# Performance work log

Measured on AMD Instinct MI355X. Metric: run time of the kernel, lower is better.

Reference implementation:

```python
import jax, jax.numpy as jnp
import numpy as np

B, I, T, H, O = 256, 128, 256, 512, 2
EPS = 1e-5  # BatchNorm1d default eps


def setup_inputs() -> dict:
    key = jax.random.key(0)
    ks = jax.random.split(key, 32)
    stdv = 1.0 / np.sqrt(H)
    u = lambda k, shape: jax.random.uniform(k, shape, jnp.float32, -stdv, stdv)
    X = jax.random.normal(ks[0], (B, I, T), jnp.float32)
    Mask = (jax.random.uniform(ks[1], (B, I, T)) > 0.5).astype(jnp.float32)
    Delta = jax.random.uniform(ks[2], (B, I, T)) * 5.0
    inp = jnp.stack([X, Mask, Delta], axis=1)  # [B, 3, I, T]
    return dict(
        input=inp,
        x_mean=jnp.float32(0.0),
        W_dg_x=u(ks[3], (I, I)), b_dg_x=u(ks[4], (I,)),
        W_dg_h=u(ks[5], (I, H)), b_dg_h=u(ks[6], (H,)),
        W_xz=u(ks[7], (I, H)), W_hz=u(ks[8], (H, H)), W_mz=u(ks[9], (I, H)), b_z=u(ks[10], (H,)),
        W_xr=u(ks[11], (I, H)), W_hr=u(ks[12], (H, H)), W_mr=u(ks[13], (I, H)), b_r=u(ks[14], (H,)),
        W_xh=u(ks[15], (I, H)), W_hh=u(ks[16], (H, H)), W_mh=u(ks[17], (I, H)), b_h=u(ks[18], (H,)),
        W_hy=u(ks[19], (H, O)), b_hy=u(ks[20], (O,)),
        bn_gamma=u(ks[21], (H,)), bn_beta=u(ks[22], (H,)),
    )


def reference(input, x_mean, W_dg_x, b_dg_x, W_dg_h, b_dg_h,
              W_xz, W_hz, W_mz, b_z, W_xr, W_hr, W_mr, b_r,
              W_xh, W_hh, W_mh, b_h, W_hy, b_hy, bn_gamma, bn_beta):
    # input: [B, 3, I, T] -> time-major [T, B, I]
    Xs = jnp.transpose(input[:, 0], (2, 0, 1))
    Ms = jnp.transpose(input[:, 1], (2, 0, 1))
    Ds = jnp.transpose(input[:, 2], (2, 0, 1))
    b, i = input.shape[0], input.shape[2]
    h0 = jnp.zeros((b, W_hz.shape[0]), input.dtype)       # Hidden_State buffer (zeros, broadcast over batch)
    xl0 = jnp.zeros((b, i), input.dtype)                   # X_last_obs buffer

    def step(carry, xs):
        h, x_last = carry
        x, m, d = xs
        gamma_x = jnp.exp(-jax.nn.relu(d @ W_dg_x + b_dg_x))   # [B, I]
        gamma_h = jnp.exp(-jax.nn.relu(d @ W_dg_h + b_dg_h))   # [B, H]
        x_last = jnp.where(m > 0, x, x_last)
        x = m * x + (1 - m) * (gamma_x * x_last + (1 - gamma_x) * x_mean)
        h = gamma_h * h
        z = jax.nn.sigmoid(x @ W_xz + h @ W_hz + m @ W_mz + b_z)
        r = jax.nn.sigmoid(x @ W_xr + h @ W_hr + m @ W_mr + b_r)
        h_tilde = jnp.tanh(x @ W_xh + (r * h) @ W_hh + m @ W_mh + b_h)
        h = (1 - z) * h + z * h_tilde
        # BatchNorm1d in training mode: batch mean, biased variance
        mu = h.mean(axis=0)
        var = ((h - mu) ** 2).mean(axis=0)
        h = bn_gamma * (h - mu) * jax.lax.rsqrt(var + EPS) + bn_beta
        y = jax.nn.softplus(h @ W_hy + b_hy)
        return (h, x_last), (y, h)

    _, (ys, hs) = jax.lax.scan(step, (h0, xl0), (Xs, Ms, Ds))
    # back to batch-major [B, T, *]
    return jnp.transpose(ys, (1, 0, 2)), jnp.transpose(hs, (1, 0, 2))
```

## Files before the change

kernel.cpp:

```cpp
#include <hip/hip_runtime.h>
#include <math.h>

#define Bb 256
#define Ii 128
#define Tt 256
#define Hh 512
#define Oo 2
#define TBr (Tt*Bb)
#define EPS_BN 1e-5f

typedef __attribute__((ext_vector_type(8))) short short8;
typedef __attribute__((ext_vector_type(8))) __bf16 bf16x8;
typedef __attribute__((ext_vector_type(4))) float f32x4;
typedef __attribute__((ext_vector_type(2))) float f32x2;
typedef unsigned long long u64;

__device__ __forceinline__ f32x4 mfma_bf16(short8 a, short8 b, f32x4 c) {
    return __builtin_amdgcn_mfma_f32_16x16x32_bf16(
        __builtin_bit_cast(bf16x8, a), __builtin_bit_cast(bf16x8, b), c, 0, 0, 0);
}
__device__ __forceinline__ short f2bf(float f) {
    union { float f; unsigned u; } v; v.f = f;
    unsigned r = (v.u + 0x7FFFu + ((v.u >> 16) & 1u)) >> 16;
    return (short)r;
}
__device__ __forceinline__ float bf2f(short s) {
    union { unsigned u; float f; } v; v.u = ((unsigned)(unsigned short)s) << 16;
    return v.f;
}
__device__ __forceinline__ float sigmoidf_(float x) { return 1.f / (1.f + expf(-x)); }
__device__ __forceinline__ float softplusf_(float x) { return fmaxf(x, 0.f) + log1pf(expf(-fabsf(x))); }

#define ALD_F(p)  __hip_atomic_load((p),  __ATOMIC_RELAXED, __HIP_MEMORY_SCOPE_AGENT)
#define AST_F(p,v) __hip_atomic_store((p), (v), __ATOMIC_RELAXED, __HIP_MEMORY_SCOPE_AGENT)
#define AADD_F(p,v) (void)__hip_atomic_fetch_add((p), (v), __ATOMIC_RELAXED, __HIP_MEMORY_SCOPE_AGENT)

__device__ __forceinline__ short8 ald16(const short* p) {
    union { u64 u[2]; short8 s; } v;
    v.u[0] = ALD_F((const u64*)p);
    v.u[1] = ALD_F((const u64*)(p + 4));
    return v.s;
}
__device__ __forceinline__ u64 pack4bf(float a, float b, float c_, float d) {
    return (u64)(unsigned short)f2bf(a)
         | ((u64)(unsigned short)f2bf(b) << 16)
         | ((u64)(unsigned short)f2bf(c_) << 32)
         | ((u64)(unsigned short)f2bf(d) << 48);
}

__global__ __launch_bounds__(1024) void repack_kernel(const float* __restrict__ in,
                                                      float* __restrict__ Xall,
                                                      short* __restrict__ Mall,
                                                      short* __restrict__ Dall)
{
    __shared__ float tile[32][33];
    const int bz = blockIdx.z;
    const int b = bz / 3, cch = bz % 3;
    const int t0 = blockIdx.x * 32, i0 = blockIdx.y * 32;
    const int tx = threadIdx.x, ty = threadIdx.y;
    const float* src = in + ((size_t)b * 3 + cch) * (size_t)Ii * Tt;
    tile[ty][tx] = src[(size_t)(i0 + ty) * Tt + t0 + tx];
    __syncthreads();
    const float v = tile[tx][ty];
    const size_t off = ((size_t)(t0 + ty) * Bb + b) * Ii + i0 + tx;
    if (cch == 0)      Xall[off] = v;
    else if (cch == 1) Mall[off] = f2bf(v);
    else               Dall[off] = f2bf(v);
}

__global__ __launch_bounds__(256) void pack_weights_kernel(
    const float* __restrict__ W_dg_x, const float* __restrict__ W_dg_h,
    const float* __restrict__ W_xz, const float* __restrict__ W_hz, const float* __restrict__ W_mz, const float* __restrict__ b_z,
    const float* __restrict__ W_xr, const float* __restrict__ W_hr, const float* __restrict__ W_mr, const float* __restrict__ b_r,
    const float* __restrict__ W_xh, const float* __restrict__ W_hh, const float* __restrict__ W_mh,
    short* __restrict__ Wc1T, short* __restrict__ Wc2T,
    short* __restrict__ WdgxT, short* __restrict__ WdghT, float* __restrict__ bias1)
{
    const int idx = blockIdx.x * blockDim.x + threadIdx.x;
    const int n1 = 1024 * 768, n2 = 512 * 768, n3 = 128 * 128, n4 = 512 * 128;
    if (idx < n1) {
        const int n = idx / 768, k = idx % 768;
        const int col = (n < Hh) ? n : (n - Hh);
        const float* Wx = (n < Hh) ? W_xz : W_xr;
        const float* Wm = (n < Hh) ? W_mz : W_mr;
        const float* Wh = (n < Hh) ? W_hz : W_hr;
        float v;
        if (k < Ii)        v = Wx[(size_t)k * Hh + col];
        else if (k < 2*Ii) v = Wm[(size_t)(k - Ii) * Hh + col];
        else               v = Wh[(size_t)(k - 2*Ii) * Hh + col];
        Wc1T[idx] = f2bf(v);
    } else if (idx < n1 + n2) {
        const int j = idx - n1;
        const int n = j / 768, k = j % 768;
        float v;
        if (k < Ii)        v = W_xh[(size_t)k * Hh + n];
        else if (k < 2*Ii) v = W_mh[(size_t)(k - Ii) * Hh + n];
        else               v = W_hh[(size_t)(k - 2*Ii) * Hh + n];
        Wc2T[j] = f2bf(v);
    } else if (idx < n1 + n2 + n3) {
        const int j = idx - n1 - n2;
        const int n = j >> 7, k = j & 127;
        WdgxT[j] = f2bf(W_dg_x[(size_t)k * Ii + n]);
    } else if (idx < n1 + n2 + n3 + n4) {
        const int j = idx - n1 - n2 - n3;
        const int n = j >> 7, k = j & 127;
        WdghT[j] = f2bf(W_dg_h[(size_t)k * Hh + n]);
    } else if (idx < n1 + n2 + n3 + n4 + 1024) {
        const int n = idx - n1 - n2 - n3 - n4;
        bias1[n] = (n < Hh) ? b_z[n] : b_r[n - Hh];
    }
}

__global__ __launch_bounds__(64) void gdecay_kernel(const short* __restrict__ A,
                                                    const short* __restrict__ BT,
                                                    const float* __restrict__ bias,
                                                    short* __restrict__ C, int N)
{
    const int lane = threadIdx.x;
    const int c = lane & 15, g = lane >> 4;
    const int m0 = blockIdx.x * 32, n0 = blockIdx.y * 64;
    const short* a0 = A + (size_t)(m0 + c) * Ii + 8 * g;
    const short* a1 = a0 + (size_t)16 * Ii;
    const short* bw = BT + (size_t)(n0 + c) * Ii + 8 * g;
    f32x4 acc[2][4];
    #pragma unroll
    for (int i = 0; i < 2; ++i)
        #pragma unroll
        for (int f = 0; f < 4; ++f) acc[i][f] = (f32x4){0.f, 0.f, 0.f, 0.f};
    #pragma unroll
    for (int k0 = 0; k0 < 128; k0 += 32) {
        const short8 av0 = *(const short8*)(a0 + k0);
        const short8 av1 = *(const short8*)(a1 + k0);
        #pragma unroll
        for (int fn = 0; fn < 4; ++fn) {
            const short8 bv = *(const short8*)(bw + (size_t)fn * 16 * Ii + k0);
            acc[0][fn] = mfma_bf16(av0, bv, acc[0][fn]);
            acc[1][fn] = mfma_bf16(av1, bv, acc[1][fn]);
        }
    }
    #pragma unroll
    for (int fn = 0; fn < 4; ++fn) {
        const int n = n0 + fn * 16 + c;
        const float bs = bias[n];
        #pragma unroll
        for (int fm = 0; fm < 2; ++fm) {
            #pragma unroll
            for (int j = 0; j < 4; ++j) {
                const int m = m0 + fm * 16 + 4 * g + j;
                const float v = expf(-fmaxf(acc[fm][fn][j] + bs, 0.f));
                C[(size_t)m * N + n] = f2bf(v);
            }
        }
    }
}

__global__ __launch_bounds__(256) void xeff_scan_kernel(const float* __restrict__ Xall,
                                                        const short* __restrict__ Mall,
                                                        const short* __restrict__ Gx,
                                                        const float* __restrict__ xmean_p,
                                                        short* __restrict__ Xe)
{
    const int bi = blockIdx.x * blockDim.x + threadIdx.x;
    if (bi >= Bb * Ii) return;
    const float xm = xmean_p[0];
    float xl = 0.f;
    for (int t = 0; t < Tt; ++t) {
        const size_t off = (size_t)t * Bb * Ii + bi;
        const float x = Xall[off];
        const float m = bf2f(Mall[off]);
        const float gx = bf2f(Gx[off]);
        if (m > 0.f) xl = x;
        Xe[off] = f2bf(m * x + (1.f - m) * (gx * xl + (1.f - gx) * xm));
    }
}

#define XM_STR 264
#define HP_STR 520
#define GH_STR 520

__global__ __launch_bounds__(512, 1) void grud_persistent(
    const short* __restrict__ Xe, const short* __restrict__ Ma,
    const short* __restrict__ Ghb,
    const short* __restrict__ Wc1T, const short* __restrict__ Wc2T,
    const float* __restrict__ bias1, const float* __restrict__ b_h,
    const float* __restrict__ bn_g, const float* __restrict__ bn_b,
    const float* __restrict__ Why, const float* __restrict__ bhy,
    short* __restrict__ rhG,
    short* __restrict__ HrawG,
    float* __restrict__ PstSum,
    int* __restrict__ f1,
    int* __restrict__ f2,
    float* __restrict__ out_hs, float* __restrict__ out_ys)
{
    const int bid = blockIdx.x, tid = threadIdx.x;
    const int w = tid >> 6, lane = tid & 63, c = lane & 15, g = lane >> 4;
    const int mt = bid & 15, ng = bid >> 4;
    const int m0 = mt * 16;

    __shared__ short sXM[16 * XM_STR];
    __shared__ short sHP[16 * HP_STR];
    __shared__ short sGH[16 * GH_STR];
    __shared__ float sZ[32 * 17];
    __shared__ float scratch[1536];
    __shared__ float sWhy[1024];
    __shared__ float scs[512], shs[512];
    __shared__ float ysred[16];

    sWhy[tid] = Why[tid]; sWhy[tid + 512] = Why[tid + 512];
    const float bhy0 = bhy[0], bhy1 = bhy[1];

    const int colt = w & 3, kh = w >> 2;
    const int colbaseA = (colt < 2) ? (ng * 32 + colt * 16)
                                    : (512 + ng * 32 + (colt - 2) * 16);
    short8 wA[12];
    {
        const short* bw = Wc1T + (size_t)(colbaseA + c) * 768 + kh * 384 + 8 * g;
        #pragma unroll
        for (int s = 0; s < 12; ++s) wA[s] = *(const short8*)(bw + 32 * s);
    }
    const int colt2 = w & 1, kq = w >> 1;
    const int colbaseB = ng * 32 + colt2 * 16;
    short8 wB[6];
    {
        const short* bw = Wc2T + (size_t)(colbaseB + c) * 768 + kq * 192 + 8 * g;
        #pragma unroll
        for (int s = 0; s < 6; ++s) wB[s] = *(const short8*)(bw + 32 * s);
    }
    {
        const int r = tid >> 5, cu = tid & 31;
        const short* src = (cu < 16)
            ? (Xe + ((size_t)(m0 + r)) * Ii + 8 * cu)
            : (Ma + ((size_t)(m0 + r)) * Ii + 8 * (cu - 16));
        *(short8*)(&sXM[r * XM_STR + 8 * cu]) = *(const short8*)src;
    }
    __syncthreads();

    for (int t = 0; t < Tt; ++t) {
        f32x4 accA = (f32x4){0.f, 0.f, 0.f, 0.f};
        f32x4 accB = (f32x4){0.f, 0.f, 0.f, 0.f};
        if (kh == 0) {
            #pragma unroll
            for (int s = 0; s < 8; ++s)
                accA = mfma_bf16(wA[s],
                    *(const short8*)(&sXM[c * XM_STR + 32 * s + 8 * g]), accA);
        }
        #pragma unroll
        for (int s = 0; s < 6; ++s) {
            const int k = kq * 192 + 32 * s;
            if (k < 256)
                accB = mfma_bf16(wB[s],
                    *(const short8*)(&sXM[c * XM_STR + k + 8 * g]), accB);
        }

        if (t > 0) {
            const int pR = (t + 2) % 3;
            {
                const float s1 = ALD_F(&PstSum[pR * 1024 + tid]);
                const float s2 = ALD_F(&PstSum[pR * 1024 + 512 + tid]);
                const float mu = s1 * (1.f / 256.f);
                const float var = fmaxf(s2 * (1.f / 256.f) - mu * mu, 0.f);
                const float sc = bn_g[tid] * rsqrtf(var + EPS_BN);
                scs[tid] = sc; shs[tid] = bn_b[tid] - mu * sc;
            }
            __syncthreads();
            float p0 = 0.f, p1 = 0.f;
            #pragma unroll
            for (int i = 0; i < 4; ++i) {
                const int idx = tid + i * 512;
                const int r = idx >> 7, c4 = (idx & 127) * 4;
                union { u64 u; unsigned short us[4]; } hv, gv;
                hv.u = ALD_F((const u64*)(HrawG + (size_t)(m0 + r) * Hh + c4));
                gv.u = *(const u64*)(&sGH[r * GH_STR + c4]);
                float h[4];
                #pragma unroll
                for (int j = 0; j < 4; ++j)
                    h[j] = fmaf(bf2f((short)hv.us[j]), scs[c4 + j], shs[c4 + j]);
                *(u64*)(&sHP[r * HP_STR + c4]) =
                    pack4bf(h[0] * bf2f((short)gv.us[0]), h[1] * bf2f((short)gv.us[1]),
                            h[2] * bf2f((short)gv.us[2]), h[3] * bf2f((short)gv.us[3]));
                if ((c4 >> 5) == ng) {
                    *(f32x4*)(&out_hs[((size_t)(m0 + r) * Tt + (t - 1)) * Hh + c4]) =
                        (f32x4){h[0], h[1], h[2], h[3]};
                }
                if (r == ng) {
                    #pragma unroll
                    for (int j = 0; j < 4; ++j) {
                        p0 = fmaf(h[j], sWhy[2 * (c4 + j)], p0);
                        p1 = fmaf(h[j], sWhy[2 * (c4 + j) + 1], p1);
                    }
                }
            }
            #pragma unroll
            for (int s = 1; s < 64; s <<= 1) { p0 += __shfl_xor(p0, s); p1 += __shfl_xor(p1, s); }
            if (lane == 0) { ysred[2 * w] = p0; ysred[2 * w + 1] = p1; }
            __syncthreads();
            if (tid == 0) {
                float q0 = 0.f, q1 = 0.f;
                #pragma unroll
                for (int i = 0; i < 8; ++i) { q0 += ysred[2 * i]; q1 += ysred[2 * i + 1]; }
                out_ys[((size_t)(m0 + ng) * Tt + (t - 1)) * Oo + 0] = softplusf_(q0 + bhy0);
                out_ys[((size_t)(m0 + ng) * Tt + (t - 1)) * Oo + 1] = softplusf_(q1 + bhy1);
            }
        } else {
            #pragma unroll
            for (int i = 0; i < 4; ++i) {
                const int idx = tid + i * 512;
                const int r = idx >> 7, c4 = (idx & 127) * 4;
                *(u64*)(&sHP[r * HP_STR + c4]) = 0ull;
            }
            __syncthreads();
        }

        if (kh == 0) {
            #pragma unroll
            for (int s = 8; s < 12; ++s)
                accA = mfma_bf16(wA[s],
                    *(const short8*)(&sHP[c * HP_STR + (32 * s - 256) + 8 * g]), accA);
        } else {
            #pragma unroll
            for (int s = 0; s < 12; ++s)
                accA = mfma_bf16(wA[s],
                    *(const short8*)(&sHP[c * HP_STR + 128 + 32 * s + 8 * g]), accA);
        }
        if (kh == 1) {
            float* sp = scratch + (colt * 64 + lane) * 4;
            sp[0] = accA[0]; sp[1] = accA[1]; sp[2] = accA[2]; sp[3] = accA[3];
        }
        __syncthreads();
        if (kh == 0) {
            const float* sp = scratch + (colt * 64 + lane) * 4;
            accA[0] += sp[0]; accA[1] += sp[1]; accA[2] += sp[2]; accA[3] += sp[3];
            if (colt < 2) {
                #pragma unroll
                for (int j = 0; j < 4; ++j) {
                    const int lc = colt * 16 + 4 * g + j;
                    const float v = sigmoidf_(accA[j] + bias1[ng * 32 + lc]);
                    sZ[lc * 17 + c] = v;
                }
            } else {
                const int nn0 = ng * 32 + (colt - 2) * 16 + 4 * g;
                float rv[4];
                #pragma unroll
                for (int j = 0; j < 4; ++j) {
                    const float v = sigmoidf_(accA[j] + bias1[512 + nn0 + j]);
                    rv[j] = v * bf2f(sHP[c * HP_STR + nn0 + j]);
                }
                AST_F((u64*)(rhG + ((size_t)(m0 + c) * Hh + nn0)),
                      pack4bf(rv[0], rv[1], rv[2], rv[3]));
            }
        }
        __syncthreads();
        if (tid == 0) AST_F(&f1[bid * 16], t + 1);
        if (t + 1 < Tt) {
            #pragma unroll
            for (int i = 0; i < 4; ++i) {
                const int idx = tid + i * 512;
                const int r = idx >> 7, c4 = (idx & 127) * 4;
                const u64 v = *(const u64*)(Ghb + ((size_t)(t + 1) * Bb + m0 + r) * Hh + c4);
                *(u64*)(&sGH[r * GH_STR + c4]) = v;
            }
        }
        if (tid < 4) AST_F(&PstSum[((t + 1) % 3) * 1024 + bid * 4 + tid], 0.f);
        if (tid < 16) {
            while (__hip_atomic_load(&f1[(mt + 16 * tid) * 16],
                                     __ATOMIC_RELAXED, __HIP_MEMORY_SCOPE_AGENT) < t + 1)
                __builtin_amdgcn_s_sleep(1);
        }
        __syncthreads();

        #pragma unroll
        for (int s = 0; s < 6; ++s) {
            const int k = kq * 192 + 32 * s;
            if (k >= 256)
                accB = mfma_bf16(wB[s],
                    ald16(rhG + (size_t)(m0 + c) * Hh + (k - 256) + 8 * g), accB);
        }
        if (kq > 0) {
            float* sp = scratch + ((colt2 * 3 + kq - 1) * 64 + lane) * 4;
            sp[0] = accB[0]; sp[1] = accB[1]; sp[2] = accB[2]; sp[3] = accB[3];
        }
        __syncthreads();
        if (kq == 0) {
            #pragma unroll
            for (int qq = 0; qq < 3; ++qq) {
                const float* sp = scratch + ((colt2 * 3 + qq) * 64 + lane) * 4;
                accB[0] += sp[0]; accB[1] += sp[1]; accB[2] += sp[2]; accB[3] += sp[3];
            }
            const int pC = t % 3;
            float hr4[4];
            #pragma unroll
            for (int j = 0; j < 4; ++j) {
                const int lc = colt2 * 16 + 4 * g + j;
                const int col = ng * 32 + lc;
                const float pre = accB[j] + b_h[col];
                const float z = sZ[lc * 17 + c];
                const float hp = bf2f(sHP[c * HP_STR + col]);
                const float hr = (1.f - z) * hp + z * tanhf(pre);
                hr4[j] = hr;
                float sp_ = hr, sq_ = hr * hr;
                sp_ += __shfl_xor(sp_, 1); sq_ += __shfl_xor(sq_, 1);
                sp_ += __shfl_xor(sp_, 2); sq_ += __shfl_xor(sq_, 2);
                sp_ += __shfl_xor(sp_, 4); sq_ += __shfl_xor(sq_, 4);
                sp_ += __shfl_xor(sp_, 8); sq_ += __shfl_xor(sq_, 8);
                if (c == 0) {
                    AADD_F(&PstSum[pC * 1024 + col], sp_);
                    AADD_F(&PstSum[pC * 1024 + 512 + col], sq_);
                }
            }
            const int cb = ng * 32 + colt2 * 16 + 4 * g;
            AST_F((u64*)(HrawG + (size_t)(m0 + c) * Hh + cb),
                  pack4bf(hr4[0], hr4[1], hr4[2], hr4[3]));
        }
        __syncthreads();
        if (tid == 0) AST_F(&f2[bid * 16], t + 1);
        if (t + 1 < Tt) {
            const int r = tid >> 5, cu = tid & 31;
            const short* src = (cu < 16)
                ? (Xe + ((size_t)(t + 1) * Bb + m0 + r) * Ii + 8 * cu)
                : (Ma + ((size_t)(t + 1) * Bb + m0 + r) * Ii + 8 * (cu - 16));
            *(short8*)(&sXM[r * XM_STR + 8 * cu]) = *(const short8*)src;
        }
        if (tid < 256) {
            while (__hip_atomic_load(&f2[tid * 16],
                                     __ATOMIC_RELAXED, __HIP_MEMORY_SCOPE_AGENT) < t + 1)
                __builtin_amdgcn_s_sleep(1);
        }
        __syncthreads();
    }

    {
        const int pR = (Tt - 1) % 3;
        {
            const float s1 = ALD_F(&PstSum[pR * 1024 + tid]);
            const float s2 = ALD_F(&PstSum[pR * 1024 + 512 + tid]);
            const float mu = s1 * (1.f / 256.f);
            const float var = fmaxf(s2 * (1.f / 256.f) - mu * mu, 0.f);
            const float sc = bn_g[tid] * rsqrtf(var + EPS_BN);
            scs[tid] = sc; shs[tid] = bn_b[tid] - mu * sc;
        }
        __syncthreads();
        float p0 = 0.f, p1 = 0.f;
        #pragma unroll
        for (int i = 0; i < 4; ++i) {
            const int idx = tid + i * 512;
            const int r = idx >> 7, c4 = (idx & 127) * 4;
            union { u64 u; unsigned short us[4]; } hv;
            hv.u = ALD_F((const u64*)(HrawG + (size_t)(m0 + r) * Hh + c4));
            float h[4];
            #pragma unroll
            for (int j = 0; j < 4; ++j)
                h[j] = fmaf(bf2f((short)hv.us[j]), scs[c4 + j], shs[c4 + j]);
            if ((c4 >> 5) == ng) {
                *(f32x4*)(&out_hs[((size_t)(m0 + r) * Tt + (Tt - 1)) * Hh + c4]) =
                    (f32x4){h[0], h[1], h[2], h[3]};
            }
            if (r == ng) {
                #pragma unroll
                for (int j = 0; j < 4; ++j) {
                    p0 = fmaf(h[j], sWhy[2 * (c4 + j)], p0);
                    p1 = fmaf(h[j], sWhy[2 * (c4 + j) + 1], p1);
                }
            }
        }
        #pragma unroll
        for (int s = 1; s < 64; s <<= 1) { p0 += __shfl_xor(p0, s); p1 += __shfl_xor(p1, s); }
        if (lane == 0) { ysred[2 * w] = p0; ysred[2 * w + 1] = p1; }
        __syncthreads();
        if (tid == 0) {
            float q0 = 0.f, q1 = 0.f;
            #pragma unroll
            for (int i = 0; i < 8; ++i) { q0 += ysred[2 * i]; q1 += ysred[2 * i + 1]; }
            out_ys[((size_t)(m0 + ng) * Tt + (Tt - 1)) * Oo + 0] = softplusf_(q0 + bhy0);
            out_ys[((size_t)(m0 + ng) * Tt + (Tt - 1)) * Oo + 1] = softplusf_(q1 + bhy1);
        }
    }
}

extern "C" void kernel_launch(void* const* d_in, const int* in_sizes, int n_in,
                              void* d_out, int out_size, void* d_ws, size_t ws_size,
                              hipStream_t stream)
{
    const float* input  = (const float*)d_in[0];
    const float* xmean  = (const float*)d_in[1];
    const float* W_dg_x = (const float*)d_in[2];
    const float* b_dg_x = (const float*)d_in[3];
    const float* W_dg_h = (const float*)d_in[4];
    const float* b_dg_h = (const float*)d_in[5];
    const float* W_xz   = (const float*)d_in[6];
    const float* W_hz   = (const float*)d_in[7];
    const float* W_mz   = (const float*)d_in[8];
    const float* b_z    = (const float*)d_in[9];
    const float* W_xr   = (const float*)d_in[10];
    const float* W_hr   = (const float*)d_in[11];
    const float* W_mr   = (const float*)d_in[12];
    const float* b_r    = (const float*)d_in[13];
    const float* W_xh   = (const float*)d_in[14];
    const float* W_hh   = (const float*)d_in[15];
    const float* W_mh   = (const float*)d_in[16];
    const float* b_h    = (const float*)d_in[17];
    const float* W_hy   = (const float*)d_in[18];
    const float* b_hy   = (const float*)d_in[19];
    const float* bn_g   = (const float*)d_in[20];
    const float* bn_b   = (const float*)d_in[21];

    float* out_ys = (float*)d_out;
    float* out_hs = out_ys + (size_t)Bb * Tt * Oo;

    char* p = (char*)d_ws;
    float* Xall = (float*)p;            p += (size_t)TBr * Ii * 4;
    short* Mall = (short*)p;            p += (size_t)TBr * Ii * 2;
    short* Dall = (short*)p;            p += (size_t)TBr * Ii * 2;
    short* Gxb  = (short*)p;            p += (size_t)TBr * Ii * 2;
    short* Ghb  = (short*)p;            p += (size_t)TBr * Hh * 2;
    short* Xe   = (short*)p;            p += (size_t)TBr * Ii * 2;
    short* Wc1T = (short*)p;            p += (size_t)1024 * 768 * 2;
    short* Wc2T = (short*)p;            p += (size_t)512 * 768 * 2;
    short* WdgxT= (short*)p;            p += (size_t)128 * 128 * 2;
    short* WdghT= (short*)p;            p += (size_t)512 * 128 * 2;
    float* bias1= (float*)p;            p += 1024 * 4;
    short* rhG  = (short*)p;            p += (size_t)Bb * Hh * 2;
    short* HrawG= (short*)p;            p += (size_t)Bb * Hh * 2;
    float* PstSum=(float*)p;            p += 3 * 1024 * 4;
    int*   f1   = (int*)p;              p += 256 * 16 * 4;
    int*   f2   = (int*)p;              p += 256 * 16 * 4;

    hipMemsetAsync(f1, 0, 256 * 16 * 4, stream);
    hipMemsetAsync(f2, 0, 256 * 16 * 4, stream);
    hipMemsetAsync(PstSum, 0, 3 * 1024 * 4, stream);

    repack_kernel<<<dim3(Tt / 32, Ii / 32, Bb * 3), dim3(32, 32), 0, stream>>>(input, Xall, Mall, Dall);

    {
        const int total = 1024 * 768 + 512 * 768 + 128 * 128 + 512 * 128 + 1024;
        pack_weights_kernel<<<(total + 255) / 256, 256, 0, stream>>>(
            W_dg_x, W_dg_h,
            W_xz, W_hz, W_mz, b_z,
            W_xr, W_hr, W_mr, b_r,
            W_xh, W_hh, W_mh,
            Wc1T, Wc2T, WdgxT, WdghT, bias1);
    }

    gdecay_kernel<<<dim3(TBr / 32, Ii / 64), 64, 0, stream>>>(Dall, WdgxT, b_dg_x, Gxb, Ii);
    gdecay_kernel<<<dim3(TBr / 32, Hh / 64), 64, 0, stream>>>(Dall, WdghT, b_dg_h, Ghb, Hh);

    xeff_scan_kernel<<<(Bb * Ii) / 256, 256, 0, stream>>>(Xall, Mall, Gxb, xmean, Xe);

    grud_persistent<<<256, 512, 0, stream>>>(
        Xe, Mall, Ghb, Wc1T, Wc2T, bias1, b_h, bn_g, bn_b,
        W_hy, b_hy, rhG, HrawG, PstSum, f1, f2, out_hs, out_ys);
}
```

Before: 2.681 ms.

## Double persistent GRU-D block to 1024 threads and split K across more waves

The persistent recurrent kernel now runs 1024 threads per block instead of 512. Each wave holds half as many weight fragments and handles a smaller K slice of the gate and candidate matmuls. Partial sums from all waves go to a larger shared scratch and are reduced by a subset of threads before the sigmoid, tanh and BatchNorm statistics. This shortens the per-step serial MFMA chain on the critical recurrent path, at the cost of more shared-memory reduction traffic, a more complex reduction, and a larger block.

```diff
diff --git a/kernel.cpp b/kernel.cpp
--- a/kernel.cpp
+++ b/kernel.cpp
@@ -12,7 +12,6 @@
 typedef __attribute__((ext_vector_type(8))) short short8;
 typedef __attribute__((ext_vector_type(8))) __bf16 bf16x8;
 typedef __attribute__((ext_vector_type(4))) float f32x4;
-typedef __attribute__((ext_vector_type(2))) float f32x2;
 typedef unsigned long long u64;
 
 __device__ __forceinline__ f32x4 mfma_bf16(short8 a, short8 b, f32x4 c) {
@@ -178,7 +177,7 @@
 #define HP_STR 520
 #define GH_STR 520
 
-__global__ __launch_bounds__(512, 1) void grud_persistent(
+__global__ __launch_bounds__(1024, 4) void grud_persistent(
     const short* __restrict__ Xe, const short* __restrict__ Ma,
     const short* __restrict__ Ghb,
     const short* __restrict__ Wc1T, const short* __restrict__ Wc2T,
@@ -201,32 +200,32 @@
     __shared__ short sHP[16 * HP_STR];
     __shared__ short sGH[16 * GH_STR];
     __shared__ float sZ[32 * 17];
-    __shared__ float scratch[1536];
+    __shared__ float scratch[4096];
     __shared__ float sWhy[1024];
     __shared__ float scs[512], shs[512];
-    __shared__ float ysred[16];
-
-    sWhy[tid] = Why[tid]; sWhy[tid + 512] = Why[tid + 512];
+    __shared__ float ysred[32];
+
+    if (tid < 512) { sWhy[tid] = Why[tid]; sWhy[tid + 512] = Why[tid + 512]; }
     const float bhy0 = bhy[0], bhy1 = bhy[1];
 
     const int colt = w & 3, kh = w >> 2;
     const int colbaseA = (colt < 2) ? (ng * 32 + colt * 16)
                                     : (512 + ng * 32 + (colt - 2) * 16);
-    short8 wA[12];
+    short8 wA[6];
     {
-        const short* bw = Wc1T + (size_t)(colbaseA + c) * 768 + kh * 384 + 8 * g;
-        #pragma unroll
-        for (int s = 0; s < 12; ++s) wA[s] = *(const short8*)(bw + 32 * s);
+        const short* bw = Wc1T + (size_t)(colbaseA + c) * 768 + kh * 192 + 8 * g;
+        #pragma unroll
+        for (int s = 0; s < 6; ++s) wA[s] = *(const short8*)(bw + 32 * s);
     }
     const int colt2 = w & 1, kq = w >> 1;
     const int colbaseB = ng * 32 + colt2 * 16;
-    short8 wB[6];
+    short8 wB[3];
     {
-        const short* bw = Wc2T + (size_t)(colbaseB + c) * 768 + kq * 192 + 8 * g;
-        #pragma unroll
-        for (int s = 0; s < 6; ++s) wB[s] = *(const short8*)(bw + 32 * s);
-    }
-    {
+        const short* bw = Wc2T + (size_t)(colbaseB + c) * 768 + kq * 96 + 8 * g;
+        #pragma unroll
+        for (int s = 0; s < 3; ++s) wB[s] = *(const short8*)(bw + 32 * s);
+    }
+    if (tid < 512) {
         const int r = tid >> 5, cu = tid & 31;
         const short* src = (cu < 16)
             ? (Xe + ((size_t)(m0 + r)) * Ii + 8 * cu)
@@ -240,21 +239,30 @@
         f32x4 accB = (f32x4){0.f, 0.f, 0.f, 0.f};
         if (kh == 0) {
             #pragma unroll
-            for (int s = 0; s < 8; ++s)
+            for (int s = 0; s < 6; ++s)
                 accA = mfma_bf16(wA[s],
                     *(const short8*)(&sXM[c * XM_STR + 32 * s + 8 * g]), accA);
-        }
-        #pragma unroll
-        for (int s = 0; s < 6; ++s) {
-            const int k = kq * 192 + 32 * s;
-            if (k < 256)
+        } else if (kh == 1) {
+            #pragma unroll
+            for (int s = 0; s < 2; ++s)
+                accA = mfma_bf16(wA[s],
+                    *(const short8*)(&sXM[c * XM_STR + 192 + 32 * s + 8 * g]), accA);
+        }
+        if (kq <= 1) {
+            #pragma unroll
+            for (int s = 0; s < 3; ++s)
                 accB = mfma_bf16(wB[s],
-                    *(const short8*)(&sXM[c * XM_STR + k + 8 * g]), accB);
+                    *(const short8*)(&sXM[c * XM_STR + kq * 96 + 32 * s + 8 * g]), accB);
+        } else if (kq == 2) {
+            #pragma unroll
+            for (int s = 0; s < 2; ++s)
+                accB = mfma_bf16(wB[s],
+                    *(const short8*)(&sXM[c * XM_STR + 192 + 32 * s + 8 * g]), accB);
         }
 
         if (t > 0) {
             const int pR = (t + 2) % 3;
-            {
+            if (tid < 512) {
                 const float s1 = ALD_F(&PstSum[pR * 1024 + tid]);
                 const float s2 = ALD_F(&PstSum[pR * 1024 + 512 + tid]);
                 const float mu = s1 * (1.f / 256.f);
@@ -265,8 +273,8 @@
             __syncthreads();
             float p0 = 0.f, p1 = 0.f;
             #pragma unroll
-            for (int i = 0; i < 4; ++i) {
-                const int idx = tid + i * 512;
+            for (int i = 0; i < 2; ++i) {
+                const int idx = tid + i * 1024;
                 const int r = idx >> 7, c4 = (idx & 127) * 4;
                 union { u64 u; unsigned short us[4]; } hv, gv;
                 hv.u = ALD_F((const u64*)(HrawG + (size_t)(m0 + r) * Hh + c4));
@@ -297,55 +305,69 @@
             if (tid == 0) {
                 float q0 = 0.f, q1 = 0.f;
                 #pragma unroll
-                for (int i = 0; i < 8; ++i) { q0 += ysred[2 * i]; q1 += ysred[2 * i + 1]; }
+                for (int i = 0; i < 16; ++i) { q0 += ysred[2 * i]; q1 += ysred[2 * i + 1]; }
                 out_ys[((size_t)(m0 + ng) * Tt + (t - 1)) * Oo + 0] = softplusf_(q0 + bhy0);
                 out_ys[((size_t)(m0 + ng) * Tt + (t - 1)) * Oo + 1] = softplusf_(q1 + bhy1);
             }
         } else {
             #pragma unroll
-            for (int i = 0; i < 4; ++i) {
-                const int idx = tid + i * 512;
+            for (int i = 0; i < 2; ++i) {
+                const int idx = tid + i * 1024;
                 const int r = idx >> 7, c4 = (idx & 127) * 4;
                 *(u64*)(&sHP[r * HP_STR + c4]) = 0ull;
             }
             __syncthreads();
         }
 
-        if (kh == 0) {
-            #pragma unroll
-            for (int s = 8; s < 12; ++s)
+        if (kh == 1) {
+            #pragma unroll
+            for (int s = 2; s < 6; ++s)
                 accA = mfma_bf16(wA[s],
-                    *(const short8*)(&sHP[c * HP_STR + (32 * s - 256) + 8 * g]), accA);
-        } else {
-            #pragma unroll
-            for (int s = 0; s < 12; ++s)
+                    *(const short8*)(&sHP[c * HP_STR + 32 * (s - 2) + 8 * g]), accA);
+        } else if (kh == 2) {
+            #pragma unroll
+            for (int s = 0; s < 6; ++s)
                 accA = mfma_bf16(wA[s],
                     *(const short8*)(&sHP[c * HP_STR + 128 + 32 * s + 8 * g]), accA);
-        }
-        if (kh == 1) {
-            float* sp = scratch + (colt * 64 + lane) * 4;
+        } else if (kh == 3) {
+            #pragma unroll
+            for (int s = 0; s < 6; ++s)
+                accA = mfma_bf16(wA[s],
+                    *(const short8*)(&sHP[c * HP_STR + 320 + 32 * s + 8 * g]), accA);
+        }
+        {
+            float* sp = scratch + tid * 4;
             sp[0] = accA[0]; sp[1] = accA[1]; sp[2] = accA[2]; sp[3] = accA[3];
         }
         __syncthreads();
-        if (kh == 0) {
-            const float* sp = scratch + (colt * 64 + lane) * 4;
-            accA[0] += sp[0]; accA[1] += sp[1]; accA[2] += sp[2]; accA[3] += sp[3];
-            if (colt < 2) {
+        if (tid < 256) {
+            const int ct = tid >> 6, rem = tid & 63;
+            const int row = rem & 15, q4 = rem >> 4;
+            const int lidx = row + 16 * q4;
+            float v4[4];
+            #pragma unroll
+            for (int j = 0; j < 4; ++j) {
+                float s = 0.f;
+                #pragma unroll
+                for (int k2 = 0; k2 < 4; ++k2)
+                    s += scratch[((k2 * 4 + ct) * 64 + lidx) * 4 + j];
+                v4[j] = s;
+            }
+            if (ct < 2) {
                 #pragma unroll
                 for (int j = 0; j < 4; ++j) {
-                    const int lc = colt * 16 + 4 * g + j;
-                    const float v = sigmoidf_(accA[j] + bias1[ng * 32 + lc]);
-                    sZ[lc * 17 + c] = v;
+                    const int lc = ct * 16 + q4 * 4 + j;
+                    sZ[lc * 17 + row] = sigmoidf_(v4[j] + bias1[ng * 32 + lc]);
                 }
             } else {
-                const int nn0 = ng * 32 + (colt - 2) * 16 + 4 * g;
+                const int nn0 = ng * 32 + (ct - 2) * 16 + q4 * 4;
                 float rv[4];
                 #pragma unroll
                 for (int j = 0; j < 4; ++j) {
-                    const float v = sigmoidf_(accA[j] + bias1[512 + nn0 + j]);
-                    rv[j] = v * bf2f(sHP[c * HP_STR + nn0 + j]);
-                }
-                AST_F((u64*)(rhG + ((size_t)(m0 + c) * Hh + nn0)),
+                    const float v = sigmoidf_(v4[j] + bias1[512 + nn0 + j]);
+                    rv[j] = v * bf2f(sHP[row * HP_STR + nn0 + j]);
+                }
+                AST_F((u64*)(rhG + ((size_t)(m0 + row) * Hh + nn0)),
                       pack4bf(rv[0], rv[1], rv[2], rv[3]));
             }
         }
@@ -353,8 +375,8 @@
         if (tid == 0) AST_F(&f1[bid * 16], t + 1);
         if (t + 1 < Tt) {
             #pragma unroll
-            for (int i = 0; i < 4; ++i) {
-                const int idx = tid + i * 512;
+            for (int i = 0; i < 2; ++i) {
+                const int idx = tid + i * 1024;
                 const int r = idx >> 7, c4 = (idx & 127) * 4;
                 const u64 v = *(const u64*)(Ghb + ((size_t)(t + 1) * Bb + m0 + r) * Hh + c4);
                 *(u64*)(&sGH[r * GH_STR + c4]) = v;
@@ -368,52 +390,62 @@
         }
         __syncthreads();
 
-        #pragma unroll
-        for (int s = 0; s < 6; ++s) {
-            const int k = kq * 192 + 32 * s;
-            if (k >= 256)
+        if (kq == 2) {
+            accB = mfma_bf16(wB[2],
+                ald16(rhG + (size_t)(m0 + c) * Hh + 8 * g), accB);
+        } else if (kq >= 3) {
+            #pragma unroll
+            for (int s = 0; s < 3; ++s)
                 accB = mfma_bf16(wB[s],
-                    ald16(rhG + (size_t)(m0 + c) * Hh + (k - 256) + 8 * g), accB);
-        }
-        if (kq > 0) {
-            float* sp = scratch + ((colt2 * 3 + kq - 1) * 64 + lane) * 4;
+                    ald16(rhG + (size_t)(m0 + c) * Hh + (kq * 96 + 32 * s - 256) + 8 * g), accB);
+        }
+        {
+            float* sp = scratch + tid * 4;
             sp[0] = accB[0]; sp[1] = accB[1]; sp[2] = accB[2]; sp[3] = accB[3];
         }
         __syncthreads();
-        if (kq == 0) {
-            #pragma unroll
-            for (int qq = 0; qq < 3; ++qq) {
-                const float* sp = scratch + ((colt2 * 3 + qq) * 64 + lane) * 4;
-                accB[0] += sp[0]; accB[1] += sp[1]; accB[2] += sp[2]; accB[3] += sp[3];
-            }
-            const int pC = t % 3;
-            float hr4[4];
+        if (tid < 128) {
+            const int row = tid & 15, q8 = tid >> 4;
+            const int c2 = q8 >> 2, q4 = q8 & 3;
+            const int lidx = row + 16 * q4;
+            float hr4[4], sp4[4], sq4[4];
             #pragma unroll
             for (int j = 0; j < 4; ++j) {
-                const int lc = colt2 * 16 + 4 * g + j;
+                float s = 0.f;
+                #pragma unroll
+                for (int k2 = 0; k2 < 8; ++k2)
+                    s += scratch[((k2 * 2 + c2) * 64 + lidx) * 4 + j];
+                const int lc = c2 * 16 + q4 * 4 + j;
                 const int col = ng * 32 + lc;
-                const float pre = accB[j] + b_h[col];
-                const float z = sZ[lc * 17 + c];
-                const float hp = bf2f(sHP[c * HP_STR + col]);
+                const float pre = s + b_h[col];
+                const float z = sZ[lc * 17 + row];
+                const float hp = bf2f(sHP[row * HP_STR + col]);
                 const float hr = (1.f - z) * hp + z * tanhf(pre);
-                hr4[j] = hr;
-                float sp_ = hr, sq_ = hr * hr;
-                sp_ += __shfl_xor(sp_, 1); sq_ += __shfl_xor(sq_, 1);
-                sp_ += __shfl_xor(sp_, 2); sq_ += __shfl_xor(sq_, 2);
-                sp_ += __shfl_xor(sp_, 4); sq_ += __shfl_xor(sq_, 4);
-                sp_ += __shfl_xor(sp_, 8); sq_ += __shfl_xor(sq_, 8);
-                if (c == 0) {
-                    AADD_F(&PstSum[pC * 1024 + col], sp_);
-                    AADD_F(&PstSum[pC * 1024 + 512 + col], sq_);
-                }
-            }
-            const int cb = ng * 32 + colt2 * 16 + 4 * g;
-            AST_F((u64*)(HrawG + (size_t)(m0 + c) * Hh + cb),
+                hr4[j] = hr; sp4[j] = hr; sq4[j] = hr * hr;
+            }
+            #pragma unroll
+            for (int j = 0; j < 4; ++j) {
+                #pragma unroll
+                for (int s = 1; s < 16; s <<= 1) {
+                    sp4[j] += __shfl_xor(sp4[j], s);
+                    sq4[j] += __shfl_xor(sq4[j], s);
+                }
+            }
+            const int cb = ng * 32 + c2 * 16 + q4 * 4;
+            AST_F((u64*)(HrawG + (size_t)(m0 + row) * Hh + cb),
                   pack4bf(hr4[0], hr4[1], hr4[2], hr4[3]));
+            if (row == 0) {
+                const int pC = t % 3;
+                #pragma unroll
+                for (int j = 0; j < 4; ++j) {
+                    AADD_F(&PstSum[pC * 1024 + cb + j], sp4[j]);
+                    AADD_F(&PstSum[pC * 1024 + 512 + cb + j], sq4[j]);
+                }
+            }
         }
         __syncthreads();
         if (tid == 0) AST_F(&f2[bid * 16], t + 1);
-        if (t + 1 < Tt) {
+        if (t + 1 < Tt && tid < 512) {
             const int r = tid >> 5, cu = tid & 31;
             const short* src = (cu < 16)
                 ? (Xe + ((size_t)(t + 1) * Bb + m0 + r) * Ii + 8 * cu)
@@ -430,7 +462,7 @@
 
     {
         const int pR = (Tt - 1) % 3;
-        {
+        if (tid < 512) {
             const float s1 = ALD_F(&PstSum[pR * 1024 + tid]);
             const float s2 = ALD_F(&PstSum[pR * 1024 + 512 + tid]);
             const float mu = s1 * (1.f / 256.f);
@@ -441,8 +473,8 @@
         __syncthreads();
         float p0 = 0.f, p1 = 0.f;
         #pragma unroll
-        for (int i = 0; i < 4; ++i) {
-            const int idx = tid + i * 512;
+        for (int i = 0; i < 2; ++i) {
+            const int idx = tid + i * 1024;
             const int r = idx >> 7, c4 = (idx & 127) * 4;
             union { u64 u; unsigned short us[4]; } hv;
             hv.u = ALD_F((const u64*)(HrawG + (size_t)(m0 + r) * Hh + c4));
@@ -469,7 +501,7 @@
         if (tid == 0) {
             float q0 = 0.f, q1 = 0.f;
             #pragma unroll
-            for (int i = 0; i < 8; ++i) { q0 += ysred[2 * i]; q1 += ysred[2 * i + 1]; }
+            for (int i = 0; i < 16; ++i) { q0 += ysred[2 * i]; q1 += ysred[2 * i + 1]; }
             out_ys[((size_t)(m0 + ng) * Tt + (Tt - 1)) * Oo + 0] = softplusf_(q0 + bhy0);
             out_ys[((size_t)(m0 + ng) * Tt + (Tt - 1)) * Oo + 1] = softplusf_(q1 + bhy1);
         }
@@ -545,7 +577,7 @@
 
     xeff_scan_kernel<<<(Bb * Ii) / 256, 256, 0, stream>>>(Xall, Mall, Gxb, xmean, Xe);
 
-    grud_persistent<<<256, 512, 0, stream>>>(
+    grud_persistent<<<256, 1024, 0, stream>>>(
         Xe, Mall, Ghb, Wc1T, Wc2T, bias1, b_h, bn_g, bn_b,
         W_hy, b_hy, rhG, HrawG, PstSum, f1, f2, out_hs, out_ys);
 }
```

After: 2.890 ms. +7.8%, slower.
